# Optimization experiments

Measured on AMD Instinct MI355X. Metric: run time of the kernel, lower is better.

## Reference

```python
import jax, jax.numpy as jnp
import numpy as np

B, N, M = 8, 8192, 1024
C1, C2 = 256, 512
C_IN, C_MID, C_OUT = 768, 256, 256  # mlp = [768, 256, 256]
EPS_BN = 1e-5
EPS_W = 1e-8


def setup_inputs() -> dict:
    key = jax.random.key(0)
    ks = jax.random.split(key, 10)
    inp = {
        "unknown": jax.random.uniform(ks[0], (B, N, 3), dtype=jnp.float32),
        "known": jax.random.uniform(ks[1], (B, M, 3), dtype=jnp.float32),
        "unknow_feats": jax.random.normal(ks[2], (B, C1, N), dtype=jnp.float32),
        "known_feats": jax.random.normal(ks[3], (B, C2, M), dtype=jnp.float32),
        # conv1d (kernel=1) weights, bias-free (followed by BN), per create_convblock1d
        "W1": jax.random.normal(ks[4], (C_MID, C_IN), dtype=jnp.float32) * (1.0 / np.sqrt(C_IN)),
        "g1": jnp.ones((C_MID,), jnp.float32),
        "b1": jnp.zeros((C_MID,), jnp.float32),
        "W2": jax.random.normal(ks[5], (C_OUT, C_MID), dtype=jnp.float32) * (1.0 / np.sqrt(C_MID)),
        "g2": jnp.ones((C_OUT,), jnp.float32),
        "b2": jnp.zeros((C_OUT,), jnp.float32),
    }
    return inp


def _three_interpolation(unknown, known, known_feats):
    # squared pairwise distances (B, N, M), as in pointnet2 three_nn CUDA kernel
    d2 = jnp.sum((unknown[:, :, None, :] - known[:, None, :, :]) ** 2, axis=-1)
    neg_d, idx = jax.lax.top_k(-d2, 3)            # (B, N, 3)
    dist = -neg_d
    w = 1.0 / (dist + EPS_W)
    w = w / jnp.sum(w, axis=-1, keepdims=True)    # (B, N, 3)
    gathered = jax.vmap(lambda f, i: f[:, i])(known_feats, idx)  # (B, C2, N, 3)
    return jnp.einsum("bcnk,bnk->bcn", gathered, w)              # (B, C2, N)


def _conv_bn_relu(x, W, g, b):
    # 1x1 conv1d (no bias) + BatchNorm1d (training-mode stats) + ReLU
    y = jnp.einsum("oc,bcn->bon", W, x)
    mean = jnp.mean(y, axis=(0, 2), keepdims=True)
    var = jnp.var(y, axis=(0, 2), keepdims=True)
    y = (y - mean) * jax.lax.rsqrt(var + EPS_BN)
    y = y * g[None, :, None] + b[None, :, None]
    return jax.nn.relu(y)


def reference(unknown, known, unknow_feats, known_feats, W1, g1, b1, W2, g2, b2):
    interp = _three_interpolation(unknown, known, known_feats)   # (B, C2, N)
    new_features = jnp.concatenate([unknow_feats, interp], axis=1)  # (B, C1+C2, N)
    h = _conv_bn_relu(new_features, W1, g1, b1)
    out = _conv_bn_relu(h, W2, g2, b2)
    return out  # (B, C_OUT, N)
```

## Files before the change

### kernel.cpp

```cpp
#include <hip/hip_runtime.h>

#define B_    8
#define N_    8192
#define M_    1024
#define C1_   256
#define C2_   512
#define CIN_  768
#define CMID_ 256
#define COUT_ 256

typedef __attribute__((ext_vector_type(8))) __bf16 bf16x8;
typedef __attribute__((ext_vector_type(4))) float f32x4;
typedef __attribute__((ext_vector_type(4))) unsigned short u16x4;
typedef __attribute__((ext_vector_type(8))) unsigned short u16x8;

__device__ __forceinline__ unsigned short f2bf(float f) {
  union { float f; unsigned u; } v; v.f = f;
  unsigned r = v.u + 0x7FFFu + ((v.u >> 16) & 1u);
  return (unsigned short)(r >> 16);
}
__device__ __forceinline__ float bf2f(unsigned short h) {
  union { unsigned u; float f; } v; v.u = ((unsigned)h) << 16; return v.f;
}

__device__ __forceinline__ void gload16(const void* g, void* l) {
  __builtin_amdgcn_global_load_lds((const __attribute__((address_space(1))) unsigned int*)g,
                                   (__attribute__((address_space(3))) unsigned int*)l, 16, 0, 0);
}


__global__ void k_cast(const float* __restrict__ in, unsigned short* __restrict__ out, int n) {
  int i = blockIdx.x * 256 + threadIdx.x;
  if (i < n) out[i] = f2bf(in[i]);
}

__global__ void k_tr_kf(const float* __restrict__ in, float* __restrict__ out) {
  __shared__ float t[32][33];
  int b = blockIdx.z;
  int c0 = blockIdx.x * 32, m0 = blockIdx.y * 32;
  int tx = threadIdx.x, ty = threadIdx.y;
  const float* ip = in + ((size_t)b * C2_ + c0) * M_ + m0;
#pragma unroll
  for (int i = 0; i < 32; i += 8) t[ty + i][tx] = ip[(size_t)(ty + i) * M_ + tx];
  __syncthreads();
  float* op = out + ((size_t)b * M_ + m0) * C2_ + c0;
#pragma unroll
  for (int i = 0; i < 32; i += 8) op[(size_t)(ty + i) * C2_ + tx] = t[tx][ty + i];
}

__global__ void k_tr_uf(const float* __restrict__ in, unsigned short* __restrict__ out) {
  __shared__ float t[32][33];
  int b = blockIdx.z;
  int c0 = blockIdx.x * 32, n0 = blockIdx.y * 32;
  int tx = threadIdx.x, ty = threadIdx.y;
  const float* ip = in + ((size_t)b * C1_ + c0) * N_ + n0;
#pragma unroll
  for (int i = 0; i < 32; i += 8) t[ty + i][tx] = ip[(size_t)(ty + i) * N_ + tx];
  __syncthreads();
  unsigned short* op = out + ((size_t)b * N_ + n0) * CIN_ + c0;
#pragma unroll
  for (int i = 0; i < 32; i += 8) op[(size_t)(ty + i) * CIN_ + tx] = f2bf(t[tx][ty + i]);
}


__device__ __forceinline__ void ins3(float db, int ib, float& d0, int& i0,
                                     float& d1, int& i1, float& d2, int& i2) {
  if (db < d2 || (db == d2 && ib < i2)) {
    if (db < d1 || (db == d1 && ib < i1)) {
      d2 = d1; i2 = i1;
      if (db < d0 || (db == d0 && ib < i0)) { d1 = d0; i1 = i0; d0 = db; i0 = ib; }
      else                                  { d1 = db; i1 = ib; }
    } else { d2 = db; i2 = ib; }
  }
}

__global__ __launch_bounds__(256) void k_three_nn(const float* __restrict__ unknown,
                                                  const float* __restrict__ known,
                                                  int* __restrict__ idx, float* __restrict__ wgt) {
  __shared__ __align__(16) float kpts[M_][4];
  int b = blockIdx.x >> 8;
  int n0 = (blockIdx.x & 255) << 5;
  for (int i = threadIdx.x; i < M_; i += 256) {
    const float* kp = known + ((size_t)b * M_ + i) * 3;
    kpts[i][0] = kp[0]; kpts[i][1] = kp[1]; kpts[i][2] = kp[2];
  }
  __syncthreads();
  const int l = threadIdx.x & 63;
  const int j = l & 7;
  const int q = ((threadIdx.x >> 6) << 3) + (l >> 3);
  const int n = n0 + q;
  const float* up = unknown + ((size_t)b * N_ + n) * 3;
  float ux = up[0], uy = up[1], uz = up[2];
  float d0 = 1e30f, d1 = 1e30f, d2v = 1e30f;
  int i0 = 0, i1 = 0, i2 = 0;
  for (int t = 0; t < 128; ++t) {
    int i = t * 8 + j;
    f32x4 p = *(const f32x4*)kpts[i];
    float dx = __fsub_rn(ux, p[0]);
    float dy = __fsub_rn(uy, p[1]);
    float dz = __fsub_rn(uz, p[2]);
    float d = __fadd_rn(__fadd_rn(__fmul_rn(dx, dx), __fmul_rn(dy, dy)), __fmul_rn(dz, dz));
    if (d < d2v) {
      if (d < d1) {
        if (d < d0) { d2v = d1; i2 = i1; d1 = d0; i1 = i0; d0 = d; i0 = i; }
        else        { d2v = d1; i2 = i1; d1 = d;  i1 = i; }
      } else        { d2v = d;  i2 = i; }
    }
  }
#pragma unroll
  for (int m = 1; m <= 4; m <<= 1) {
    float e0 = __shfl_xor(d0, m), e1 = __shfl_xor(d1, m), e2 = __shfl_xor(d2v, m);
    int   f0 = __shfl_xor(i0, m), f1 = __shfl_xor(i1, m), f2 = __shfl_xor(i2, m);
    ins3(e0, f0, d0, i0, d1, i1, d2v, i2);
    ins3(e1, f1, d0, i0, d1, i1, d2v, i2);
    ins3(e2, f2, d0, i0, d1, i1, d2v, i2);
  }
  if (j == 0) {
    float w0 = 1.f / (d0 + 1e-8f), w1 = 1.f / (d1 + 1e-8f), w2 = 1.f / (d2v + 1e-8f);
    float s = w0 + w1 + w2;
    size_t base = ((size_t)b * N_ + n) * 3;
    idx[base] = i0; idx[base + 1] = i1; idx[base + 2] = i2;
    wgt[base] = w0 / s; wgt[base + 1] = w1 / s; wgt[base + 2] = w2 / s;
  }
}

__global__ __launch_bounds__(256) void k_interp(const float* __restrict__ kft, const int* __restrict__ idx,
                                                const float* __restrict__ wgt, unsigned short* __restrict__ xt) {
  int pb = blockIdx.x * 8 + (threadIdx.x >> 5);
  int lane = threadIdx.x & 31;
  int b = pb >> 13;
  size_t t3 = (size_t)pb * 3;
  int i0 = idx[t3], i1 = idx[t3 + 1], i2 = idx[t3 + 2];
  float w0 = wgt[t3], w1 = wgt[t3 + 1], w2 = wgt[t3 + 2];
  const f32x4* f0 = (const f32x4*)(kft + ((size_t)b * M_ + i0) * C2_);
  const f32x4* f1 = (const f32x4*)(kft + ((size_t)b * M_ + i1) * C2_);
  const f32x4* f2 = (const f32x4*)(kft + ((size_t)b * M_ + i2) * C2_);
  unsigned short* o = xt + (size_t)pb * CIN_ + C1_;
#pragma unroll
  for (int k = 0; k < 4; ++k) {
    int c4 = lane + 32 * k;
    f32x4 a = f0[c4], bb = f1[c4], cc = f2[c4];
    u16x4 r;
#pragma unroll
    for (int e = 0; e < 4; ++e) r[e] = f2bf(w0 * a[e] + w1 * bb[e] + w2 * cc[e]);
    *(u16x4*)(o + 4 * c4) = r;
  }
}


template <int K, int EPI, bool BN>
__global__ __launch_bounds__(256, 4) void gemm_bt(const unsigned short* __restrict__ A,
                                                  const unsigned short* __restrict__ Bm,
                                                  unsigned short* __restrict__ C,
                                                  float* __restrict__ psum, float* __restrict__ psq,
                                                  const float* __restrict__ scale,
                                                  const float* __restrict__ shift) {
  __shared__ __align__(16) char lds[36864];
  float* lsc = (float*)(lds + 32768);
  float* lsh = (float*)(lds + 33792);
  const int tid = threadIdx.x;
  const int l = tid & 63;
  const int wv = tid >> 6;
  const int wr = wv >> 1, wc = wv & 1;
  const int b = blockIdx.z;
  const int o0 = blockIdx.y * 128;
  const int n0 = blockIdx.x * 128;
  const char* Ab = (const char*)A + (size_t)o0 * (K * 2);
  const char* Bb = (const char*)Bm + ((size_t)b * N_ + n0) * (K * 2);

  if (BN) {
    lsc[tid] = scale[tid]; lsh[tid] = shift[tid];
    __syncthreads();
  }

  f32x4 acc[4][4];
#pragma unroll
  for (int i = 0; i < 4; ++i)
#pragma unroll
    for (int j = 0; j < 4; ++j) acc[i][j] = f32x4{0.f, 0.f, 0.f, 0.f};

  const int grow = wv * 32 + (l >> 2);
  const int gcol = ((l & 3) ^ ((l >> 3) & 3)) * 16;
  int srow[2], sg[2];
#pragma unroll
  for (int i = 0; i < 2; ++i) { int q = tid + i * 256; srow[i] = q >> 2; sg[i] = q & 3; }

  auto issueA = [&](int kt, char* buf) {
#pragma unroll
    for (int i = 0; i < 2; ++i)
      gload16(Ab + (size_t)(grow + i * 16) * (K * 2) + kt * 64 + gcol,
              buf + wv * 2048 + i * 1024);
  };
  auto issueB = [&](int kt, char* buf) {
#pragma unroll
    for (int i = 0; i < 2; ++i)
      gload16(Bb + (size_t)(grow + i * 16) * (K * 2) + kt * 64 + gcol,
              buf + 8192 + wv * 2048 + i * 1024);
  };
  auto loadBreg = [&](bf16x8* rb, int kt) {
#pragma unroll
    for (int i = 0; i < 2; ++i)
      rb[i] = *(const bf16x8*)(Bb + (size_t)srow[i] * (K * 2) + kt * 64 + sg[i] * 16);
  };
  auto bnwrite = [&](bf16x8* rb, int kt, char* buf) {
#pragma unroll
    for (int i = 0; i < 2; ++i) {
      u16x8 v = *(u16x8*)&rb[i];
      int c0 = kt * 32 + sg[i] * 8;
      u16x8 r;
#pragma unroll
      for (int e = 0; e < 8; ++e)
        r[e] = f2bf(fmaxf(bf2f(v[e]) * lsc[c0 + e] + lsh[c0 + e], 0.f));
      *(u16x8*)(buf + 8192 + srow[i] * 64 + (sg[i] ^ ((srow[i] >> 1) & 3)) * 16) = r;
    }
  };

  if (BN) {
    bf16x8 rb0[2];
    loadBreg(rb0, 0);
    issueA(0, lds);
    bnwrite(rb0, 0, lds);
  } else {
    issueA(0, lds);
    issueB(0, lds);
  }
  __syncthreads();

  const int NK = K / 32;
  int cur = 0;
  for (int kt = 0; kt < NK; ++kt) {
    const bool haveNext = (kt + 1 < NK);
    char* nb = lds + (cur ^ 1) * 16384;
    bf16x8 rb2[2];
    if (haveNext) {
      if (BN) { loadBreg(rb2, kt + 1); issueA(kt + 1, nb); }
      else    { issueA(kt + 1, nb); issueB(kt + 1, nb); }
    }
    const char* base = lds + cur * 16384;
    bf16x8 af[4], bfr[4];
#pragma unroll
    for (int mi = 0; mi < 4; ++mi) {
      int row = wr * 64 + mi * 16 + (l & 15);
      int g = (l >> 4) ^ ((row >> 1) & 3);
      af[mi] = *(const bf16x8*)(base + row * 64 + g * 16);
    }
#pragma unroll
    for (int ni = 0; ni < 4; ++ni) {
      int row = wc * 64 + ni * 16 + (l & 15);
      int g = (l >> 4) ^ ((row >> 1) & 3);
      bfr[ni] = *(const bf16x8*)(base + 8192 + row * 64 + g * 16);
    }
#pragma unroll
    for (int mi = 0; mi < 4; ++mi)
#pragma unroll
      for (int ni = 0; ni < 4; ++ni)
        acc[mi][ni] = __builtin_amdgcn_mfma_f32_16x16x32_bf16(af[mi], bfr[ni], acc[mi][ni], 0, 0, 0);
    if (BN && haveNext) bnwrite(rb2, kt + 1, nb);
    __syncthreads();
    cur ^= 1;
  }

  const int slot = (blockIdx.z * 64 + blockIdx.x) * 2 + wc;
#pragma unroll
  for (int mi = 0; mi < 4; ++mi) {
    float s[4] = {0.f, 0.f, 0.f, 0.f}, q[4] = {0.f, 0.f, 0.f, 0.f};
#pragma unroll
    for (int ni = 0; ni < 4; ++ni)
#pragma unroll
      for (int r = 0; r < 4; ++r) { float v = acc[mi][ni][r]; s[r] += v; q[r] = fmaf(v, v, q[r]); }
#pragma unroll
    for (int m = 1; m <= 8; m <<= 1)
#pragma unroll
      for (int r = 0; r < 4; ++r) { s[r] += __shfl_xor(s[r], m); q[r] += __shfl_xor(q[r], m); }
    if ((l & 15) == 0) {
      int o = o0 + wr * 64 + mi * 16 + ((l >> 4) << 2);
#pragma unroll
      for (int r = 0; r < 4; ++r) {
        psum[(size_t)(o + r) * 1024 + slot] = s[r];
        psq [(size_t)(o + r) * 1024 + slot] = q[r];
      }
    }
  }

  unsigned short* t16 = (unsigned short*)lds;
#pragma unroll
  for (int mi = 0; mi < 4; ++mi) {
    int ol = wr * 64 + mi * 16 + ((l >> 4) << 2);
#pragma unroll
    for (int ni = 0; ni < 4; ++ni) {
      int nl = wc * 64 + ni * 16 + (l & 15);
#pragma unroll
      for (int r = 0; r < 4; ++r) {
        unsigned short v = f2bf(acc[mi][ni][r]);
        if (EPI == 0) t16[nl * 144 + ol + r] = v;
        else          t16[(ol + r) * 144 + nl] = v;
      }
    }
  }
  __syncthreads();
#pragma unroll
  for (int t = 0; t < 8; ++t) {
    int row = wv * 32 + (l >> 4) + t * 4;
    u16x8 v = *(const u16x8*)(t16 + row * 144 + (l & 15) * 8);
    if (EPI == 0)
      *(u16x8*)(C + ((size_t)b * N_ + n0 + row) * 256 + o0 + (l & 15) * 8) = v;
    else
      *(u16x8*)(C + ((size_t)b * 256 + o0 + row) * N_ + n0 + (l & 15) * 8) = v;
  }
}


__global__ __launch_bounds__(256) void k_finalize(const float* __restrict__ psum,
                                                  const float* __restrict__ psq,
                                                  const float* __restrict__ g,
                                                  const float* __restrict__ bb,
                                                  float* __restrict__ scale,
                                                  float* __restrict__ shift) {
  int c = blockIdx.x;
  const float* ps = psum + (size_t)c * 1024;
  const float* pq = psq + (size_t)c * 1024;
  float s = 0.f, q = 0.f;
#pragma unroll
  for (int k = 0; k < 4; ++k) { s += ps[threadIdx.x + 256 * k]; q += pq[threadIdx.x + 256 * k]; }
#pragma unroll
  for (int off = 32; off; off >>= 1) { s += __shfl_down(s, off); q += __shfl_down(q, off); }
  __shared__ float rs[4], rq[4];
  if ((threadIdx.x & 63) == 0) { rs[threadIdx.x >> 6] = s; rq[threadIdx.x >> 6] = q; }
  __syncthreads();
  if (threadIdx.x == 0) {
    float S = rs[0] + rs[1] + rs[2] + rs[3];
    float Q = rq[0] + rq[1] + rq[2] + rq[3];
    const float inv_n = 1.f / 65536.f;
    float mean = S * inv_n;
    float var = Q * inv_n - mean * mean;
    float rstd = rsqrtf(var + 1e-5f);
    float sc = g[c] * rstd;
    scale[c] = sc;
    shift[c] = bb[c] - mean * sc;
  }
}

__global__ void k_bnrelu_out(const unsigned short* __restrict__ y, const float* __restrict__ scale,
                             const float* __restrict__ shift, float* __restrict__ out) {
  size_t i = ((size_t)blockIdx.x * 256 + threadIdx.x) * 4;
  int c = (int)((i >> 13) & 255);
  float sc = scale[c], sh = shift[c];
  u16x4 v = *(const u16x4*)(y + i);
  f32x4 o;
#pragma unroll
  for (int k = 0; k < 4; ++k) o[k] = fmaxf(bf2f(v[k]) * sc + sh, 0.f);
  *(f32x4*)(out + i) = o;
}


extern "C" void kernel_launch(void* const* d_in, const int* in_sizes, int n_in,
                              void* d_out, int out_size, void* d_ws, size_t ws_size,
                              hipStream_t stream) {
  const float* unknown = (const float*)d_in[0];
  const float* known   = (const float*)d_in[1];
  const float* uf      = (const float*)d_in[2];
  const float* kf      = (const float*)d_in[3];
  const float* W1      = (const float*)d_in[4];
  const float* g1      = (const float*)d_in[5];
  const float* b1      = (const float*)d_in[6];
  const float* W2      = (const float*)d_in[7];
  const float* g2      = (const float*)d_in[8];
  const float* b2      = (const float*)d_in[9];
  float* out = (float*)d_out;

  char* ws = (char*)d_ws;
  unsigned short* xt  = (unsigned short*)(ws);
  unsigned short* y1  = (unsigned short*)(ws + 100663296);
  unsigned short* y2  = (unsigned short*)(ws + 134217728);
  float*          kft = (float*)(ws + 167772160);
  float*          psum = (float*)(ws + 167772160);
  float*          psq  = (float*)(ws + 168820736);
  unsigned short* w1b = (unsigned short*)(ws + 184549376);
  unsigned short* w2b = (unsigned short*)(ws + 184942592);
  int*            idx = (int*)(ws + 185073664);
  float*          wgt = (float*)(ws + 185860096);
  float*          st  = (float*)(ws + 186646528);
  float *sc1 = st, *sh1 = st + 256, *sc2 = st + 512, *sh2 = st + 768;

  k_cast<<<768, 256, 0, stream>>>(W1, w1b, CMID_ * CIN_);
  k_cast<<<256, 256, 0, stream>>>(W2, w2b, COUT_ * CMID_);
  k_tr_kf<<<dim3(16, 32, B_), dim3(32, 8), 0, stream>>>(kf, kft);
  k_tr_uf<<<dim3(8, 256, B_), dim3(32, 8), 0, stream>>>(uf, xt);
  k_three_nn<<<B_ * 256, 256, 0, stream>>>(unknown, known, idx, wgt);
  k_interp<<<B_ * N_ / 8, 256, 0, stream>>>(kft, idx, wgt, xt);
  gemm_bt<CIN_, 0, false><<<dim3(64, 2, B_), 256, 0, stream>>>(w1b, xt, y1, psum, psq, nullptr, nullptr);
  k_finalize<<<256, 256, 0, stream>>>(psum, psq, g1, b1, sc1, sh1);
  gemm_bt<CMID_, 1, true><<<dim3(64, 2, B_), 256, 0, stream>>>(w2b, y1, y2, psum, psq, sc1, sh1);
  k_finalize<<<256, 256, 0, stream>>>(psum, psq, g2, b2, sc2, sh2);
  k_bnrelu_out<<<16384, 256, 0, stream>>>(y2, sc2, sh2, out);
}
```

Measured before the change: 205.8 us.

## Widen GEMM tiles to cover all 256 output channels per block

Each GEMM block now computes all 256 output channels for its 128-column tile instead of splitting channels across two blocks in grid y. The B operand, which holds the activations and for the second GEMM also the fused BN+ReLU transform, is loaded and transformed once instead of twice. To fit, each wave keeps twice as many accumulators, LDS grows to 50 KB, launch bounds drop to 2 blocks per CU, and the epilogue writes out in two passes. Occupancy falls, the grid halves to 512 blocks, and register pressure rises.

New measurement: 198.0 us. 1.04x faster.

```diff
diff --git a/kernel.cpp b/kernel.cpp
--- a/kernel.cpp
+++ b/kernel.cpp
@@ -149,23 +149,22 @@
 
 
 template <int K, int EPI, bool BN>
-__global__ __launch_bounds__(256, 4) void gemm_bt(const unsigned short* __restrict__ A,
+__global__ __launch_bounds__(256, 2) void gemm_bt(const unsigned short* __restrict__ A,
                                                   const unsigned short* __restrict__ Bm,
                                                   unsigned short* __restrict__ C,
                                                   float* __restrict__ psum, float* __restrict__ psq,
                                                   const float* __restrict__ scale,
                                                   const float* __restrict__ shift) {
-  __shared__ __align__(16) char lds[36864];
-  float* lsc = (float*)(lds + 32768);
-  float* lsh = (float*)(lds + 33792);
+  __shared__ __align__(16) char lds[51200];
+  float* lsc = (float*)(lds + 49152);
+  float* lsh = (float*)(lds + 50176);
   const int tid = threadIdx.x;
   const int l = tid & 63;
   const int wv = tid >> 6;
   const int wr = wv >> 1, wc = wv & 1;
-  const int b = blockIdx.z;
-  const int o0 = blockIdx.y * 128;
+  const int b = blockIdx.y;
   const int n0 = blockIdx.x * 128;
-  const char* Ab = (const char*)A + (size_t)o0 * (K * 2);
+  const char* Ab = (const char*)A;
   const char* Bb = (const char*)Bm + ((size_t)b * N_ + n0) * (K * 2);
 
   if (BN) {
@@ -173,13 +172,12 @@
     __syncthreads();
   }
 
-  f32x4 acc[4][4];
-#pragma unroll
-  for (int i = 0; i < 4; ++i)
+  f32x4 acc[8][4];
+#pragma unroll
+  for (int i = 0; i < 8; ++i)
 #pragma unroll
     for (int j = 0; j < 4; ++j) acc[i][j] = f32x4{0.f, 0.f, 0.f, 0.f};
 
-  const int grow = wv * 32 + (l >> 2);
   const int gcol = ((l & 3) ^ ((l >> 3) & 3)) * 16;
   int srow[2], sg[2];
 #pragma unroll
@@ -187,15 +185,15 @@
 
   auto issueA = [&](int kt, char* buf) {
 #pragma unroll
-    for (int i = 0; i < 2; ++i)
-      gload16(Ab + (size_t)(grow + i * 16) * (K * 2) + kt * 64 + gcol,
-              buf + wv * 2048 + i * 1024);
+    for (int i = 0; i < 4; ++i)
+      gload16(Ab + (size_t)(wv * 64 + i * 16 + (l >> 2)) * (K * 2) + kt * 64 + gcol,
+              buf + wv * 4096 + i * 1024);
   };
   auto issueB = [&](int kt, char* buf) {
 #pragma unroll
     for (int i = 0; i < 2; ++i)
-      gload16(Bb + (size_t)(grow + i * 16) * (K * 2) + kt * 64 + gcol,
-              buf + 8192 + wv * 2048 + i * 1024);
+      gload16(Bb + (size_t)(wv * 32 + i * 16 + (l >> 2)) * (K * 2) + kt * 64 + gcol,
+              buf + 16384 + wv * 2048 + i * 1024);
   };
   auto loadBreg = [&](bf16x8* rb, int kt) {
 #pragma unroll
@@ -211,7 +209,7 @@
 #pragma unroll
       for (int e = 0; e < 8; ++e)
         r[e] = f2bf(fmaxf(bf2f(v[e]) * lsc[c0 + e] + lsh[c0 + e], 0.f));
-      *(u16x8*)(buf + 8192 + srow[i] * 64 + (sg[i] ^ ((srow[i] >> 1) & 3)) * 16) = r;
+      *(u16x8*)(buf + 16384 + srow[i] * 64 + (sg[i] ^ ((srow[i] >> 1) & 3)) * 16) = r;
     }
   };
 
@@ -230,17 +228,17 @@
   int cur = 0;
   for (int kt = 0; kt < NK; ++kt) {
     const bool haveNext = (kt + 1 < NK);
-    char* nb = lds + (cur ^ 1) * 16384;
+    char* nb = lds + (cur ^ 1) * 24576;
     bf16x8 rb2[2];
     if (haveNext) {
       if (BN) { loadBreg(rb2, kt + 1); issueA(kt + 1, nb); }
       else    { issueA(kt + 1, nb); issueB(kt + 1, nb); }
     }
-    const char* base = lds + cur * 16384;
-    bf16x8 af[4], bfr[4];
-#pragma unroll
-    for (int mi = 0; mi < 4; ++mi) {
-      int row = wr * 64 + mi * 16 + (l & 15);
+    const char* base = lds + cur * 24576;
+    bf16x8 af[8], bfr[4];
+#pragma unroll
+    for (int mi = 0; mi < 8; ++mi) {
+      int row = wr * 128 + mi * 16 + (l & 15);
       int g = (l >> 4) ^ ((row >> 1) & 3);
       af[mi] = *(const bf16x8*)(base + row * 64 + g * 16);
     }
@@ -248,10 +246,10 @@
     for (int ni = 0; ni < 4; ++ni) {
       int row = wc * 64 + ni * 16 + (l & 15);
       int g = (l >> 4) ^ ((row >> 1) & 3);
-      bfr[ni] = *(const bf16x8*)(base + 8192 + row * 64 + g * 16);
-    }
-#pragma unroll
-    for (int mi = 0; mi < 4; ++mi)
+      bfr[ni] = *(const bf16x8*)(base + 16384 + row * 64 + g * 16);
+    }
+#pragma unroll
+    for (int mi = 0; mi < 8; ++mi)
 #pragma unroll
       for (int ni = 0; ni < 4; ++ni)
         acc[mi][ni] = __builtin_amdgcn_mfma_f32_16x16x32_bf16(af[mi], bfr[ni], acc[mi][ni], 0, 0, 0);
@@ -260,9 +258,9 @@
     cur ^= 1;
   }
 
-  const int slot = (blockIdx.z * 64 + blockIdx.x) * 2 + wc;
-#pragma unroll
-  for (int mi = 0; mi < 4; ++mi) {
+  const int slot = (b * 64 + blockIdx.x) * 2 + wc;
+#pragma unroll
+  for (int mi = 0; mi < 8; ++mi) {
     float s[4] = {0.f, 0.f, 0.f, 0.f}, q[4] = {0.f, 0.f, 0.f, 0.f};
 #pragma unroll
     for (int ni = 0; ni < 4; ++ni)
@@ -273,7 +271,7 @@
 #pragma unroll
       for (int r = 0; r < 4; ++r) { s[r] += __shfl_xor(s[r], m); q[r] += __shfl_xor(q[r], m); }
     if ((l & 15) == 0) {
-      int o = o0 + wr * 64 + mi * 16 + ((l >> 4) << 2);
+      int o = wr * 128 + mi * 16 + ((l >> 4) << 2);
 #pragma unroll
       for (int r = 0; r < 4; ++r) {
         psum[(size_t)(o + r) * 1024 + slot] = s[r];
@@ -284,28 +282,34 @@
 
   unsigned short* t16 = (unsigned short*)lds;
 #pragma unroll
-  for (int mi = 0; mi < 4; ++mi) {
-    int ol = wr * 64 + mi * 16 + ((l >> 4) << 2);
-#pragma unroll
-    for (int ni = 0; ni < 4; ++ni) {
-      int nl = wc * 64 + ni * 16 + (l & 15);
-#pragma unroll
-      for (int r = 0; r < 4; ++r) {
-        unsigned short v = f2bf(acc[mi][ni][r]);
-        if (EPI == 0) t16[nl * 144 + ol + r] = v;
-        else          t16[(ol + r) * 144 + nl] = v;
+  for (int p = 0; p < 2; ++p) {
+    __syncthreads();
+    if (wr == p) {
+#pragma unroll
+      for (int mi = 0; mi < 8; ++mi) {
+        int ol = mi * 16 + ((l >> 4) << 2);
+#pragma unroll
+        for (int ni = 0; ni < 4; ++ni) {
+          int nl = wc * 64 + ni * 16 + (l & 15);
+#pragma unroll
+          for (int r = 0; r < 4; ++r) {
+            unsigned short v = f2bf(acc[mi][ni][r]);
+            if (EPI == 0) t16[nl * 144 + ol + r] = v;
+            else          t16[(ol + r) * 144 + nl] = v;
+          }
+        }
       }
     }
-  }
-  __syncthreads();
-#pragma unroll
-  for (int t = 0; t < 8; ++t) {
-    int row = wv * 32 + (l >> 4) + t * 4;
-    u16x8 v = *(const u16x8*)(t16 + row * 144 + (l & 15) * 8);
-    if (EPI == 0)
-      *(u16x8*)(C + ((size_t)b * N_ + n0 + row) * 256 + o0 + (l & 15) * 8) = v;
-    else
-      *(u16x8*)(C + ((size_t)b * 256 + o0 + row) * N_ + n0 + (l & 15) * 8) = v;
+    __syncthreads();
+#pragma unroll
+    for (int t = 0; t < 8; ++t) {
+      int row = wv * 32 + (l >> 4) + t * 4;
+      u16x8 v = *(const u16x8*)(t16 + row * 144 + (l & 15) * 8);
+      if (EPI == 0)
+        *(u16x8*)(C + ((size_t)b * N_ + n0 + row) * 256 + p * 128 + (l & 15) * 8) = v;
+      else
+        *(u16x8*)(C + ((size_t)b * 256 + p * 128 + row) * N_ + n0 + (l & 15) * 8) = v;
+    }
   }
 }
 
@@ -388,9 +392,9 @@
   k_tr_uf<<<dim3(8, 256, B_), dim3(32, 8), 0, stream>>>(uf, xt);
   k_three_nn<<<B_ * 256, 256, 0, stream>>>(unknown, known, idx, wgt);
   k_interp<<<B_ * N_ / 8, 256, 0, stream>>>(kft, idx, wgt, xt);
-  gemm_bt<CIN_, 0, false><<<dim3(64, 2, B_), 256, 0, stream>>>(w1b, xt, y1, psum, psq, nullptr, nullptr);
+  gemm_bt<CIN_, 0, false><<<dim3(64, B_), 256, 0, stream>>>(w1b, xt, y1, psum, psq, nullptr, nullptr);
   k_finalize<<<256, 256, 0, stream>>>(psum, psq, g1, b1, sc1, sh1);
-  gemm_bt<CMID_, 1, true><<<dim3(64, 2, B_), 256, 0, stream>>>(w2b, y1, y2, psum, psq, sc1, sh1);
+  gemm_bt<CMID_, 1, true><<<dim3(64, B_), 256, 0, stream>>>(w2b, y1, y2, psum, psq, sc1, sh1);
   k_finalize<<<256, 256, 0, stream>>>(psum, psq, g2, b2, sc2, sh2);
   k_bnrelu_out<<<16384, 256, 0, stream>>>(y2, sc2, sh2, out);
 }
```
